# Performance work log

Measured on AMD Instinct MI355X. Metric: run time of the kernel, lower is better.

Reference implementation:

```python
import jax, jax.numpy as jnp
import numpy as np

D_MODEL = 1024
NUM_HEADS = 16
D_HEAD = D_MODEL // NUM_HEADS


def setup_inputs() -> dict:
    key = jax.random.key(0)
    ks = jax.random.split(key, 10)
    B, L = 2, 2048
    s = 1.0 / np.sqrt(D_MODEL)
    inp = {
        'x_q': jax.random.normal(ks[0], (B, L, D_MODEL), jnp.float32),
        'x_kv': jax.random.normal(ks[1], (B, L, D_MODEL), jnp.float32),
        'wq': jax.random.normal(ks[2], (D_MODEL, D_MODEL), jnp.float32) * s,
        'bq': jnp.zeros((D_MODEL,), jnp.float32),
        'wk': jax.random.normal(ks[3], (D_MODEL, D_MODEL), jnp.float32) * s,
        'bk': jnp.zeros((D_MODEL,), jnp.float32),
        'wv': jax.random.normal(ks[4], (D_MODEL, D_MODEL), jnp.float32) * s,
        'bv': jnp.zeros((D_MODEL,), jnp.float32),
        'wo': jax.random.normal(ks[5], (D_MODEL, D_MODEL), jnp.float32) * s,
        'bo': jnp.zeros((D_MODEL,), jnp.float32),
    }
    return inp


def _split_heads(x):
    B, L, _ = x.shape
    return x.reshape(B, L, NUM_HEADS, D_HEAD).transpose(0, 2, 1, 3)  # (B,H,L,Dh)


def reference(x_q, x_kv, wq, bq, wk, bk, wv, bv, wo, bo):
    # Linear projections (torch Linear: x @ W^T + b)
    q = _split_heads(x_q @ wq.T + bq)   # (B,H,Lq,Dh)
    k = _split_heads(x_kv @ wk.T + bk)  # (B,H,Lk,Dh)
    v = _split_heads(x_kv @ wv.T + bv)  # (B,H,Lk,Dh)
    scale = 1.0 / jnp.sqrt(jnp.asarray(D_HEAD, q.dtype))
    scores = jnp.einsum('bhqd,bhkd->bhqk', q, k) * scale
    attn = jax.nn.softmax(scores, axis=-1)
    out = jnp.einsum('bhqk,bhkd->bhqd', attn, v)  # (B,H,Lq,Dh)
    B, H, Lq, Dh = out.shape
    out = out.transpose(0, 2, 1, 3).reshape(B, Lq, H * Dh)
    # dropout is identity in eval mode
    return out @ wo.T + bo
```

## Files before the change

### kernel.cpp

```cpp
#include <hip/hip_runtime.h>
#include <hip/hip_bf16.h>

typedef _Float16 __attribute__((ext_vector_type(8))) half8;
typedef _Float16 __attribute__((ext_vector_type(4))) half4;
typedef __fp16 __attribute__((ext_vector_type(2))) fp16x2;
typedef __fp16 __attribute__((ext_vector_type(4))) fp16x4;
typedef float __attribute__((ext_vector_type(4))) f32x4;

typedef __attribute__((address_space(1))) void gvoid_t;
typedef __attribute__((address_space(3))) void lvoid_t;

__device__ __forceinline__ void gld_lds16(const void* g, void* l) {
    __builtin_amdgcn_global_load_lds((const gvoid_t*)g, (lvoid_t*)l, 16, 0, 0);
}

__global__ void cvt_all(const float* __restrict__ x_q, const float* __restrict__ x_kv,
                        const float* __restrict__ wq, const float* __restrict__ wk,
                        const float* __restrict__ wv, const float* __restrict__ wo,
                        _Float16* __restrict__ xq16, _Float16* __restrict__ xkv16,
                        _Float16* __restrict__ wq16, _Float16* __restrict__ wk16,
                        _Float16* __restrict__ wv16, _Float16* __restrict__ wo16)
{
    const int y = blockIdx.y;
    const int n = (y < 2) ? (4096 * 1024) : (1024 * 1024);
    int i = (blockIdx.x * 256 + threadIdx.x) * 8;
    if (i >= n) return;
    const float* in = (y == 0) ? x_q : (y == 1) ? x_kv : (y == 2) ? wq : (y == 3) ? wk : (y == 4) ? wv : wo;
    _Float16* out = (y == 0) ? xq16 : (y == 1) ? xkv16 : (y == 2) ? wq16 : (y == 3) ? wk16 : (y == 4) ? wv16 : wo16;
    float4 a = *(const float4*)(in + i);
    float4 b = *(const float4*)(in + i + 4);
    half8 h;
    h[0] = (_Float16)a.x; h[1] = (_Float16)a.y; h[2] = (_Float16)a.z; h[3] = (_Float16)a.w;
    h[4] = (_Float16)b.x; h[5] = (_Float16)b.y; h[6] = (_Float16)b.z; h[7] = (_Float16)b.w;
    *(half8*)(out + i) = h;
}

template <typename OutT, bool VT>
__device__ __forceinline__ void gemm_body(
    const _Float16* __restrict__ A,
    const _Float16* __restrict__ W,
    const float* __restrict__ bias,
    OutT* __restrict__ C,
    int N, int K, int bm, int bn, float osc,
    _Float16* As, _Float16* Bs)
{
    const int tid = threadIdx.x;
    const int wv = tid >> 6;
    const int lane = tid & 63;
    const int lr = lane & 15;
    const int lk = lane >> 4;
    const int wm = wv >> 1, wn = wv & 1;

    f32x4 acc[2][4] = {};

    for (int k0 = 0; k0 < K; k0 += 64) {
        __syncthreads();
#pragma unroll
        for (int i = 0; i < 2; ++i) {
            int chunk = i * 256 + tid;
            int row = chunk >> 3, c8 = chunk & 7;
            gld_lds16(A + (size_t)(bm * 64 + row) * K + k0 + c8 * 8, &As[chunk * 8]);
        }
#pragma unroll
        for (int i = 0; i < 4; ++i) {
            int chunk = i * 256 + tid;
            int row = chunk >> 3, c8 = chunk & 7;
            gld_lds16(W + (size_t)(bn * 128 + row) * K + k0 + c8 * 8, &Bs[chunk * 8]);
        }
        __syncthreads();

#pragma unroll
        for (int kk = 0; kk < 2; ++kk) {
            half8 a[2], b[4];
#pragma unroll
            for (int m = 0; m < 2; ++m)
                a[m] = *(const half8*)&As[(wm * 32 + m * 16 + lr) * 64 + kk * 32 + lk * 8];
#pragma unroll
            for (int n = 0; n < 4; ++n)
                b[n] = *(const half8*)&Bs[(wn * 64 + n * 16 + lr) * 64 + kk * 32 + lk * 8];
#pragma unroll
            for (int m = 0; m < 2; ++m)
#pragma unroll
                for (int n = 0; n < 4; ++n)
                    acc[m][n] = __builtin_amdgcn_mfma_f32_16x16x32_f16(a[m], b[n], acc[m][n], 0, 0, 0);
        }
    }

#pragma unroll
    for (int m = 0; m < 2; ++m) {
#pragma unroll
        for (int n = 0; n < 4; ++n) {
            int row0 = bm * 64 + wm * 32 + m * 16 + lk * 4;
            int col  = bn * 128 + wn * 64 + n * 16 + lr;
            float bb = bias[col];
            if (VT) {
                int b = row0 >> 11, l0 = row0 & 2047, h = col >> 6, dh = col & 63;
                half4 hv;
#pragma unroll
                for (int r = 0; r < 4; ++r) hv[r] = (_Float16)((acc[m][n][r] + bb) * osc);
                *(half4*)&C[(size_t)(((b * 16 + h) * 64 + dh)) * 2048 + l0] = hv;
            } else {
#pragma unroll
                for (int r = 0; r < 4; ++r) {
                    float v = (acc[m][n][r] + bb) * osc;
                    C[(size_t)(row0 + r) * N + col] = (OutT)v;
                }
            }
        }
    }
}

template <typename OutT>
__global__ __launch_bounds__(256) void gemm_bt(
    const _Float16* __restrict__ A, const _Float16* __restrict__ W,
    const float* __restrict__ bias, OutT* __restrict__ C,
    int M, int N, int K)
{
    __shared__ _Float16 As[64 * 64];
    __shared__ _Float16 Bs[128 * 64];
    const int nbn = N >> 7;
    gemm_body<OutT, false>(A, W, bias, C, N, K, blockIdx.x / nbn, blockIdx.x % nbn, 1.0f, As, Bs);
}

__global__ __launch_bounds__(256) void gemm_qkv(
    const _Float16* __restrict__ xq, const _Float16* __restrict__ xkv,
    const _Float16* __restrict__ wqp, const _Float16* __restrict__ wkp, const _Float16* __restrict__ wvp,
    const float* __restrict__ bq, const float* __restrict__ bk, const float* __restrict__ bvv,
    _Float16* __restrict__ Qb, _Float16* __restrict__ Kb, _Float16* __restrict__ VbT)
{
    __shared__ _Float16 As[64 * 64];
    __shared__ _Float16 Bs[128 * 64];
    const int z = blockIdx.y;
    const _Float16* A = (z == 0) ? xq : xkv;
    const _Float16* W = (z == 0) ? wqp : (z == 1) ? wkp : wvp;
    const float* bias = (z == 0) ? bq : (z == 1) ? bk : bvv;
    const int bm = blockIdx.x >> 3, bn = blockIdx.x & 7;
    if (z == 2)
        gemm_body<_Float16, true>(A, W, bias, VbT, 1024, 1024, bm, bn, 1.0f, As, Bs);
    else
        gemm_body<_Float16, false>(A, W, bias, (z == 0) ? Qb : Kb, 1024, 1024, bm, bn,
                                   (z == 0) ? (0.125f * 1.44269504088896f) : 1.0f, As, Bs);
}

__global__ __launch_bounds__(512, 4) void attn_fwd(
    const _Float16* __restrict__ Q,
    const _Float16* __restrict__ Kt,
    const _Float16* __restrict__ VT,
    _Float16* __restrict__ O)
{
    constexpr int KT = 128;
    __shared__ __align__(16) _Float16 Ks[KT * 64];
    __shared__ __align__(16) _Float16 Vs[64 * KT];

    const int tid = threadIdx.x;
    const int wv = tid >> 6;
    const int lane = tid & 63;
    const int lr = lane & 15;
    const int lk = lane >> 4;
    const int qb = blockIdx.x;
    const int bh = blockIdx.y;
    const size_t base = (size_t)(bh >> 4) * (2048 * 1024) + (size_t)(bh & 15) * 64;
    const size_t vtbase = (size_t)bh * (64 * 2048);

    half8 qf[2];
    {
        const _Float16* qp = Q + base + (size_t)(qb * 128 + wv * 16 + lr) * 1024 + lk * 8;
        qf[0] = *(const half8*)qp;
        qf[1] = *(const half8*)(qp + 32);
    }

    const _Float16* kb0 = &Ks[lr * 64 + ((lk     ^ (lr & 7)) << 3)];
    const _Float16* kb1 = &Ks[lr * 64 + (((4|lk) ^ (lr & 7)) << 3)];
    const _Float16* vb[8];
#pragma unroll
    for (int kvb = 0; kvb < 8; ++kvb)
        vb[kvb] = &Vs[lr * 128 + ((((kvb << 1) | (lk >> 1)) ^ lr) << 3) + ((lk & 1) << 2)];

    float mr = -1e30f, ls = 0.f;
    f32x4 o[4] = {};

    for (int kt = 0; kt < 2048; kt += KT) {
        __syncthreads();
#pragma unroll
        for (int i = 0; i < 2; ++i) {
            int chunk = i * 512 + tid;
            int row = chunk >> 3, c8 = chunk & 7;
            int c8s = c8 ^ (row & 7);
            gld_lds16(Kt + base + (size_t)(kt + row) * 1024 + c8s * 8, &Ks[chunk * 8]);
        }
#pragma unroll
        for (int i = 0; i < 2; ++i) {
            int chunk = i * 512 + tid;
            int row = chunk >> 4, c16 = chunk & 15;
            int c16s = c16 ^ (row & 15);
            gld_lds16(VT + vtbase + (size_t)row * 2048 + kt + c16s * 8, &Vs[chunk * 8]);
        }
        __syncthreads();

        f32x4 s[8] = {};
#pragma unroll
        for (int n = 0; n < 8; ++n) {
            half8 a0 = *(const half8*)(kb0 + n * 1024);
            s[n] = __builtin_amdgcn_mfma_f32_16x16x32_f16(a0, qf[0], s[n], 0, 0, 0);
        }
#pragma unroll
        for (int n = 0; n < 8; ++n) {
            half8 a1 = *(const half8*)(kb1 + n * 1024);
            s[n] = __builtin_amdgcn_mfma_f32_16x16x32_f16(a1, qf[1], s[n], 0, 0, 0);
        }

        float tm = -1e30f;
#pragma unroll
        for (int n = 0; n < 8; ++n)
#pragma unroll
            for (int r = 0; r < 4; ++r) tm = fmaxf(tm, s[n][r]);
        tm = fmaxf(tm, __shfl_xor(tm, 16));
        tm = fmaxf(tm, __shfl_xor(tm, 32));

        if (!__all(tm <= mr + 8.0f)) {
            float mn = fmaxf(mr, tm);
            float al = __builtin_amdgcn_exp2f(mr - mn);
            mr = mn;
            ls *= al;
#pragma unroll
            for (int nd = 0; nd < 4; ++nd)
#pragma unroll
                for (int r = 0; r < 4; ++r) o[nd][r] *= al;
        }

        float rs = 0.f;
        half4 pf[8];
#pragma unroll
        for (int n = 0; n < 8; ++n) {
            float p0 = __builtin_amdgcn_exp2f(s[n][0] - mr);
            float p1 = __builtin_amdgcn_exp2f(s[n][1] - mr);
            float p2 = __builtin_amdgcn_exp2f(s[n][2] - mr);
            float p3 = __builtin_amdgcn_exp2f(s[n][3] - mr);
            rs += (p0 + p1) + (p2 + p3);
            fp16x2 lo = __builtin_amdgcn_cvt_pkrtz(p0, p1);
            fp16x2 hi = __builtin_amdgcn_cvt_pkrtz(p2, p3);
            fp16x4 pv4 = __builtin_shufflevector(lo, hi, 0, 1, 2, 3);
            pf[n] = __builtin_bit_cast(half4, pv4);
        }
        rs += __shfl_xor(rs, 16);
        rs += __shfl_xor(rs, 32);
        ls += rs;

#pragma unroll
        for (int kvb = 0; kvb < 8; ++kvb) {
#pragma unroll
            for (int nd = 0; nd < 4; ++nd) {
                half4 va = *(const half4*)(vb[kvb] + nd * 2048);
                o[nd] = __builtin_amdgcn_mfma_f32_16x16x16f16(va, pf[kvb], o[nd], 0, 0, 0);
            }
        }
    }

    const float inv = 1.0f / ls;
    const size_t orow = base + (size_t)(qb * 128 + wv * 16 + lr) * 1024;
#pragma unroll
    for (int nd = 0; nd < 4; ++nd) {
        half4 hv;
#pragma unroll
        for (int r = 0; r < 4; ++r) hv[r] = (_Float16)(o[nd][r] * inv);
        *(half4*)&O[orow + nd * 16 + lk * 4] = hv;
    }
}

extern "C" void kernel_launch(void* const* d_in, const int* in_sizes, int n_in,
                              void* d_out, int out_size, void* d_ws, size_t ws_size,
                              hipStream_t stream) {
    const float* x_q  = (const float*)d_in[0];
    const float* x_kv = (const float*)d_in[1];
    const float* wq   = (const float*)d_in[2];
    const float* bq   = (const float*)d_in[3];
    const float* wk   = (const float*)d_in[4];
    const float* bk   = (const float*)d_in[5];
    const float* wvp  = (const float*)d_in[6];
    const float* bv   = (const float*)d_in[7];
    const float* wo   = (const float*)d_in[8];
    const float* bo   = (const float*)d_in[9];
    float* out = (float*)d_out;

    const size_t MX = (size_t)4096 * 1024;
    const size_t WX = (size_t)1024 * 1024;
    _Float16* ws    = (_Float16*)d_ws;
    _Float16* xq16  = ws;
    _Float16* xkv16 = xq16 + MX;
    _Float16* wq16  = xkv16 + MX;
    _Float16* wk16  = wq16 + WX;
    _Float16* wv16  = wk16 + WX;
    _Float16* wo16  = wv16 + WX;
    _Float16* Qb    = wo16 + WX;
    _Float16* Kb    = Qb + MX;
    _Float16* VbT   = Kb + MX;
    _Float16* AO    = VbT + MX;

    cvt_all<<<dim3(2048, 6), 256, 0, stream>>>(x_q, x_kv, wq, wk, wvp, wo,
                                               xq16, xkv16, wq16, wk16, wv16, wo16);

    gemm_qkv<<<dim3(512, 3), 256, 0, stream>>>(xq16, xkv16, wq16, wk16, wv16,
                                               bq, bk, bv, Qb, Kb, VbT);

    attn_fwd<<<dim3(16, 32), 512, 0, stream>>>(Qb, Kb, VbT, AO);

    gemm_bt<float><<<dim3(512), 256, 0, stream>>>(AO, wo16, bo, out, 4096, 1024, 1024);
}
```

Measured before the change: 141.0 us.

## Double-buffer LDS tiles in GEMM and attention, remap attention block order

Both the GEMM body and the attention kernel now keep two LDS buffers, issuing the async global-to-LDS loads for the next K tile before computing on the current one. This cuts the per-iteration double barrier down to a single barrier and aims to hide global load latency behind MFMA work. Attention also moves to a 1D grid with a swizzled block index that spreads consecutive blocks across heads, intended to improve cache or XCD locality. LDS usage doubles, which can reduce occupancy, especially for the attention kernel launched with 512 threads and a min-blocks bound of 4.

Result: no change. 138.9 us (-1.5%).

```diff
diff --git a/kernel.cpp b/kernel.cpp
--- a/kernel.cpp
+++ b/kernel.cpp
@@ -51,38 +51,47 @@
     const int lk = lane >> 4;
     const int wm = wv >> 1, wn = wv & 1;
 
-    f32x4 acc[2][4] = {};
-
-    for (int k0 = 0; k0 < K; k0 += 64) {
-        __syncthreads();
+    auto stage = [&](int cb, int k0) {
 #pragma unroll
         for (int i = 0; i < 2; ++i) {
             int chunk = i * 256 + tid;
             int row = chunk >> 3, c8 = chunk & 7;
-            gld_lds16(A + (size_t)(bm * 64 + row) * K + k0 + c8 * 8, &As[chunk * 8]);
+            gld_lds16(A + (size_t)(bm * 64 + row) * K + k0 + c8 * 8, &As[cb * 4096 + chunk * 8]);
         }
 #pragma unroll
         for (int i = 0; i < 4; ++i) {
             int chunk = i * 256 + tid;
             int row = chunk >> 3, c8 = chunk & 7;
-            gld_lds16(W + (size_t)(bn * 128 + row) * K + k0 + c8 * 8, &Bs[chunk * 8]);
-        }
-        __syncthreads();
-
-#pragma unroll
-        for (int kk = 0; kk < 2; ++kk) {
-            half8 a[2], b[4];
-#pragma unroll
-            for (int m = 0; m < 2; ++m)
-                a[m] = *(const half8*)&As[(wm * 32 + m * 16 + lr) * 64 + kk * 32 + lk * 8];
-#pragma unroll
-            for (int n = 0; n < 4; ++n)
-                b[n] = *(const half8*)&Bs[(wn * 64 + n * 16 + lr) * 64 + kk * 32 + lk * 8];
-#pragma unroll
-            for (int m = 0; m < 2; ++m)
+            gld_lds16(W + (size_t)(bn * 128 + row) * K + k0 + c8 * 8, &Bs[cb * 8192 + chunk * 8]);
+        }
+    };
+
+    f32x4 acc[2][4] = {};
+
+    stage(0, 0);
+    __syncthreads();
+
+    for (int k2 = 0; k2 < K; k2 += 128) {
+#pragma unroll
+        for (int hf = 0; hf < 2; ++hf) {
+            const int k0 = k2 + hf * 64;
+            if (k0 + 64 < K) stage(hf ^ 1, k0 + 64);
+#pragma unroll
+            for (int kk = 0; kk < 2; ++kk) {
+                half8 a[2], b[4];
+#pragma unroll
+                for (int m = 0; m < 2; ++m)
+                    a[m] = *(const half8*)&As[hf * 4096 + (wm * 32 + m * 16 + lr) * 64 + kk * 32 + lk * 8];
 #pragma unroll
                 for (int n = 0; n < 4; ++n)
-                    acc[m][n] = __builtin_amdgcn_mfma_f32_16x16x32_f16(a[m], b[n], acc[m][n], 0, 0, 0);
+                    b[n] = *(const half8*)&Bs[hf * 8192 + (wn * 64 + n * 16 + lr) * 64 + kk * 32 + lk * 8];
+#pragma unroll
+                for (int m = 0; m < 2; ++m)
+#pragma unroll
+                    for (int n = 0; n < 4; ++n)
+                        acc[m][n] = __builtin_amdgcn_mfma_f32_16x16x32_f16(a[m], b[n], acc[m][n], 0, 0, 0);
+            }
+            __syncthreads();
         }
     }
 
@@ -116,8 +125,8 @@
     const float* __restrict__ bias, OutT* __restrict__ C,
     int M, int N, int K)
 {
-    __shared__ _Float16 As[64 * 64];
-    __shared__ _Float16 Bs[128 * 64];
+    __shared__ _Float16 As[2 * 64 * 64];
+    __shared__ _Float16 Bs[2 * 128 * 64];
     const int nbn = N >> 7;
     gemm_body<OutT, false>(A, W, bias, C, N, K, blockIdx.x / nbn, blockIdx.x % nbn, 1.0f, As, Bs);
 }
@@ -128,8 +137,8 @@
     const float* __restrict__ bq, const float* __restrict__ bk, const float* __restrict__ bvv,
     _Float16* __restrict__ Qb, _Float16* __restrict__ Kb, _Float16* __restrict__ VbT)
 {
-    __shared__ _Float16 As[64 * 64];
-    __shared__ _Float16 Bs[128 * 64];
+    __shared__ _Float16 As[2 * 64 * 64];
+    __shared__ _Float16 Bs[2 * 128 * 64];
     const int z = blockIdx.y;
     const _Float16* A = (z == 0) ? xq : xkv;
     const _Float16* W = (z == 0) ? wqp : (z == 1) ? wkp : wvp;
@@ -149,16 +158,17 @@
     _Float16* __restrict__ O)
 {
     constexpr int KT = 128;
-    __shared__ __align__(16) _Float16 Ks[KT * 64];
-    __shared__ __align__(16) _Float16 Vs[64 * KT];
+    __shared__ __align__(16) _Float16 Ks[2][KT * 64];
+    __shared__ __align__(16) _Float16 Vs[2][64 * KT];
 
     const int tid = threadIdx.x;
     const int wv = tid >> 6;
     const int lane = tid & 63;
     const int lr = lane & 15;
     const int lk = lane >> 4;
-    const int qb = blockIdx.x;
-    const int bh = blockIdx.y;
+    const int id = ((blockIdx.x & 7) << 6) | (blockIdx.x >> 3);
+    const int qb = id & 15;
+    const int bh = id >> 4;
     const size_t base = (size_t)(bh >> 4) * (2048 * 1024) + (size_t)(bh & 15) * 64;
     const size_t vtbase = (size_t)bh * (64 * 2048);
 
@@ -169,90 +179,100 @@
         qf[1] = *(const half8*)(qp + 32);
     }
 
-    const _Float16* kb0 = &Ks[lr * 64 + ((lk     ^ (lr & 7)) << 3)];
-    const _Float16* kb1 = &Ks[lr * 64 + (((4|lk) ^ (lr & 7)) << 3)];
-    const _Float16* vb[8];
-#pragma unroll
-    for (int kvb = 0; kvb < 8; ++kvb)
-        vb[kvb] = &Vs[lr * 128 + ((((kvb << 1) | (lk >> 1)) ^ lr) << 3) + ((lk & 1) << 2)];
-
-    float mr = -1e30f, ls = 0.f;
-    f32x4 o[4] = {};
-
-    for (int kt = 0; kt < 2048; kt += KT) {
-        __syncthreads();
+    auto stage = [&](int cb, int kt) {
 #pragma unroll
         for (int i = 0; i < 2; ++i) {
             int chunk = i * 512 + tid;
             int row = chunk >> 3, c8 = chunk & 7;
             int c8s = c8 ^ (row & 7);
-            gld_lds16(Kt + base + (size_t)(kt + row) * 1024 + c8s * 8, &Ks[chunk * 8]);
+            gld_lds16(Kt + base + (size_t)(kt + row) * 1024 + c8s * 8, &Ks[cb][chunk * 8]);
         }
 #pragma unroll
         for (int i = 0; i < 2; ++i) {
             int chunk = i * 512 + tid;
             int row = chunk >> 4, c16 = chunk & 15;
             int c16s = c16 ^ (row & 15);
-            gld_lds16(VT + vtbase + (size_t)row * 2048 + kt + c16s * 8, &Vs[chunk * 8]);
-        }
-        __syncthreads();
-
-        f32x4 s[8] = {};
-#pragma unroll
-        for (int n = 0; n < 8; ++n) {
-            half8 a0 = *(const half8*)(kb0 + n * 1024);
-            s[n] = __builtin_amdgcn_mfma_f32_16x16x32_f16(a0, qf[0], s[n], 0, 0, 0);
-        }
-#pragma unroll
-        for (int n = 0; n < 8; ++n) {
-            half8 a1 = *(const half8*)(kb1 + n * 1024);
-            s[n] = __builtin_amdgcn_mfma_f32_16x16x32_f16(a1, qf[1], s[n], 0, 0, 0);
-        }
-
-        float tm = -1e30f;
-#pragma unroll
-        for (int n = 0; n < 8; ++n)
-#pragma unroll
-            for (int r = 0; r < 4; ++r) tm = fmaxf(tm, s[n][r]);
-        tm = fmaxf(tm, __shfl_xor(tm, 16));
-        tm = fmaxf(tm, __shfl_xor(tm, 32));
-
-        if (!__all(tm <= mr + 8.0f)) {
-            float mn = fmaxf(mr, tm);
-            float al = __builtin_amdgcn_exp2f(mr - mn);
-            mr = mn;
-            ls *= al;
-#pragma unroll
-            for (int nd = 0; nd < 4; ++nd)
-#pragma unroll
-                for (int r = 0; r < 4; ++r) o[nd][r] *= al;
-        }
-
-        float rs = 0.f;
-        half4 pf[8];
-#pragma unroll
-        for (int n = 0; n < 8; ++n) {
-            float p0 = __builtin_amdgcn_exp2f(s[n][0] - mr);
-            float p1 = __builtin_amdgcn_exp2f(s[n][1] - mr);
-            float p2 = __builtin_amdgcn_exp2f(s[n][2] - mr);
-            float p3 = __builtin_amdgcn_exp2f(s[n][3] - mr);
-            rs += (p0 + p1) + (p2 + p3);
-            fp16x2 lo = __builtin_amdgcn_cvt_pkrtz(p0, p1);
-            fp16x2 hi = __builtin_amdgcn_cvt_pkrtz(p2, p3);
-            fp16x4 pv4 = __builtin_shufflevector(lo, hi, 0, 1, 2, 3);
-            pf[n] = __builtin_bit_cast(half4, pv4);
-        }
-        rs += __shfl_xor(rs, 16);
-        rs += __shfl_xor(rs, 32);
-        ls += rs;
-
-#pragma unroll
-        for (int kvb = 0; kvb < 8; ++kvb) {
-#pragma unroll
-            for (int nd = 0; nd < 4; ++nd) {
-                half4 va = *(const half4*)(vb[kvb] + nd * 2048);
-                o[nd] = __builtin_amdgcn_mfma_f32_16x16x16f16(va, pf[kvb], o[nd], 0, 0, 0);
-            }
+            gld_lds16(VT + vtbase + (size_t)row * 2048 + kt + c16s * 8, &Vs[cb][chunk * 8]);
+        }
+    };
+
+    float mr = -1e30f, ls = 0.f;
+    f32x4 o[4] = {};
+
+    stage(0, 0);
+    __syncthreads();
+
+    for (int kt2 = 0; kt2 < 2048; kt2 += 2 * KT) {
+#pragma unroll
+        for (int hf = 0; hf < 2; ++hf) {
+            const int kt = kt2 + hf * KT;
+            if (kt + KT < 2048) stage(hf ^ 1, kt + KT);
+
+            const _Float16* kb0 = &Ks[hf][lr * 64 + ((lk     ^ (lr & 7)) << 3)];
+            const _Float16* kb1 = &Ks[hf][lr * 64 + (((4|lk) ^ (lr & 7)) << 3)];
+            const _Float16* vbb = &Vs[hf][lr * 128 + ((lk & 1) << 2)];
+
+            f32x4 s[8] = {};
+#pragma unroll
+            for (int n = 0; n < 8; ++n) {
+                half8 a0 = *(const half8*)(kb0 + n * 1024);
+                s[n] = __builtin_amdgcn_mfma_f32_16x16x32_f16(a0, qf[0], s[n], 0, 0, 0);
+            }
+#pragma unroll
+            for (int n = 0; n < 8; ++n) {
+                half8 a1 = *(const half8*)(kb1 + n * 1024);
+                s[n] = __builtin_amdgcn_mfma_f32_16x16x32_f16(a1, qf[1], s[n], 0, 0, 0);
+            }
+
+            float tm = -1e30f;
+#pragma unroll
+            for (int n = 0; n < 8; ++n)
+#pragma unroll
+                for (int r = 0; r < 4; ++r) tm = fmaxf(tm, s[n][r]);
+            tm = fmaxf(tm, __shfl_xor(tm, 16));
+            tm = fmaxf(tm, __shfl_xor(tm, 32));
+
+            if (!__all(tm <= mr + 8.0f)) {
+                float mn = fmaxf(mr, tm);
+                float al = __builtin_amdgcn_exp2f(mr - mn);
+                mr = mn;
+                ls *= al;
+#pragma unroll
+                for (int nd = 0; nd < 4; ++nd)
+#pragma unroll
+                    for (int r = 0; r < 4; ++r) o[nd][r] *= al;
+            }
+
+            float rs = 0.f;
+            half4 pf[8];
+#pragma unroll
+            for (int n = 0; n < 8; ++n) {
+                float p0 = __builtin_amdgcn_exp2f(s[n][0] - mr);
+                float p1 = __builtin_amdgcn_exp2f(s[n][1] - mr);
+                float p2 = __builtin_amdgcn_exp2f(s[n][2] - mr);
+                float p3 = __builtin_amdgcn_exp2f(s[n][3] - mr);
+                rs += (p0 + p1) + (p2 + p3);
+                fp16x2 lo = __builtin_amdgcn_cvt_pkrtz(p0, p1);
+                fp16x2 hi = __builtin_amdgcn_cvt_pkrtz(p2, p3);
+                fp16x4 pv4 = __builtin_shufflevector(lo, hi, 0, 1, 2, 3);
+                pf[n] = __builtin_bit_cast(half4, pv4);
+            }
+            rs += __shfl_xor(rs, 16);
+            rs += __shfl_xor(rs, 32);
+            ls += rs;
+
+#pragma unroll
+            for (int kvb = 0; kvb < 8; ++kvb) {
+                int co = ((((kvb << 1) | (lk >> 1)) ^ lr) << 3) - (lr << 3);
+#pragma unroll
+                for (int nd = 0; nd < 4; ++nd) {
+                    half4 va = *(const half4*)&Vs[hf][lr * 128 + ((((kvb << 1) | (lk >> 1)) ^ lr) << 3) + ((lk & 1) << 2) + nd * 2048];
+                    o[nd] = __builtin_amdgcn_mfma_f32_16x16x16f16(va, pf[kvb], o[nd], 0, 0, 0);
+                }
+            }
+            (void)vbb;
+
+            __syncthreads();
         }
     }
 
@@ -302,7 +322,7 @@
     gemm_qkv<<<dim3(512, 3), 256, 0, stream>>>(xq16, xkv16, wq16, wk16, wv16,
                                                bq, bk, bv, Qb, Kb, VbT);
 
-    attn_fwd<<<dim3(16, 32), 512, 0, stream>>>(Qb, Kb, VbT, AO);
+    attn_fwd<<<dim3(512), 512, 0, stream>>>(Qb, Kb, VbT, AO);
 
     gemm_bt<float><<<dim3(512), 256, 0, stream>>>(AO, wo16, bo, out, 4096, 1024, 1024);
 }
```
